# Kernel tuning notes

Measured on AMD Instinct MI355X. Metric: run time of the kernel, lower is better.

Reference implementation:

```python
import jax, jax.numpy as jnp
import numpy as np

N_USERS = 60000
N_ITEMS = 40000
N = N_USERS + N_ITEMS   # ncount
EMB = 64
NNZ = 3200000           # nnz of sparse_norm_adj (avg degree 32)
LN_EPS = 1e-5


def setup_inputs() -> dict:
    key = jax.random.key(0)
    ks = jax.random.split(key, 12)
    ego = jax.random.normal(ks[0], (N, EMB), jnp.float32) * 0.1
    rows = jax.random.randint(ks[1], (NNZ,), 0, N)
    cols = jax.random.randint(ks[2], (NNZ,), 0, N)
    # normalized adjacency values (non-trainable buffer)
    vals = jax.random.uniform(ks[3], (NNZ,), jnp.float32) * 0.01
    # xavier-uniform-ish scale for [64,64]: sqrt(2/(64+64)) = 0.125
    w_uu = jax.random.normal(ks[4], (EMB, EMB), jnp.float32) * 0.125
    filt_uu = jax.random.uniform(ks[5], (N_USERS,), jnp.float32, 0.99, 1.01)
    par_uu = jax.random.uniform(ks[6], (2,), jnp.float32, 0.0, 0.99)
    w_ii = jax.random.normal(ks[7], (EMB, EMB), jnp.float32) * 0.125
    filt_ii = jax.random.uniform(ks[8], (N_ITEMS,), jnp.float32, 0.99, 1.01)
    par_ii = jax.random.uniform(ks[9], (2,), jnp.float32, 0.0, 0.99)
    ln_gamma = jnp.ones((EMB,), jnp.float32)
    ln_beta = jnp.zeros((EMB,), jnp.float32)
    return {"ego_embeddings": ego, "rows": rows, "cols": cols, "vals": vals,
            "w_uu": w_uu, "filt_uu": filt_uu, "par_uu": par_uu,
            "w_ii": w_ii, "filt_ii": filt_ii, "par_ii": par_ii,
            "ln_gamma": ln_gamma, "ln_beta": ln_beta}


def _spmm(rows, cols, vals, x):
    # out[rows] += vals * x[cols]  <=>  sparse_adj @ x
    return jax.ops.segment_sum(vals[:, None] * x[cols], rows, num_segments=N)


def reference(ego_embeddings, rows, cols, vals, w_uu, filt_uu, par_uu,
              w_ii, filt_ii, par_ii, ln_gamma, ln_beta):
    res = ego_embeddings
    u = ego_embeddings[:N_USERS]
    it = ego_embeddings[N_USERS:]
    # HWNN layer with K1=K2=1 collapses to par0*par1 * diag(filter) @ X @ W
    user_ego = par_uu[0] * par_uu[1] * ((filt_uu[:, None] * u) @ w_uu) + u
    item_ego = par_ii[0] * par_ii[1] * ((filt_ii[:, None] * it) @ w_ii) + it
    ego = jnp.concatenate([user_ego, item_ego], axis=0)  # [N, EMB]
    # HGCNConv (act=False): adj @ (adj.T @ ego)
    h = jax.ops.segment_sum(vals[:, None] * ego[rows], cols, num_segments=N)  # adj.T @ ego
    y = _spmm(rows, cols, vals, h)                                            # adj @ h
    # LayerNorm (eps=1e-5, affine) + residual from the ORIGINAL input
    mu = jnp.mean(y, axis=-1, keepdims=True)
    var = jnp.var(y, axis=-1, keepdims=True)
    yn = (y - mu) / jnp.sqrt(var + LN_EPS) * ln_gamma + ln_beta
    out = yn + res
    return out[:N_USERS], out[N_USERS:]
```

## Files before the change

kernel.cpp:

```cpp
#include <hip/hip_runtime.h>

#define N_USERS 60000
#define N_ITEMS 40000
#define N_TOTAL 100000
#define EMB 64
#define LN_EPS 1e-5f

#define KPS 128
#define KSH 7
#define NSUP ((N_TOTAL + KPS - 1) / KPS)
#define EPB 4096
#define BLT 512
#define TR_ROWS 32
#define XPITCH 68
#define CAP 2048
#define SPT 512

__device__ __forceinline__ float bf2f(unsigned short h)
{ return __uint_as_float(((unsigned)h) << 16); }
__device__ __forceinline__ unsigned short f2bf(float f)
{
    unsigned u = __float_as_uint(f);
    return (unsigned short)((u + 0x7FFFu + ((u >> 16) & 1u)) >> 16);
}

__global__ void transform_tile(const float* __restrict__ x,
                               const float* __restrict__ w_uu,
                               const float* __restrict__ filt_uu,
                               const float* __restrict__ par_uu,
                               const float* __restrict__ w_ii,
                               const float* __restrict__ filt_ii,
                               const float* __restrict__ par_ii,
                               unsigned short* __restrict__ out)
{
    __shared__ float Wls[EMB * EMB];
    __shared__ float xs[TR_ROWS * XPITCH];
    const int tid = threadIdx.x;
    const int r0 = blockIdx.x * TR_ROWS;
    const int itm = (r0 >= N_USERS);
    const float* W  = itm ? w_ii : w_uu;
    const float* fb = itm ? filt_ii : filt_uu;
    const int foff  = itm ? N_USERS : 0;
    const float c   = itm ? par_ii[0] * par_ii[1] : par_uu[0] * par_uu[1];

    for (int i = tid; i < EMB * EMB / 4; i += 256)
        ((float4*)Wls)[i] = ((const float4*)W)[i];
    for (int i = tid; i < TR_ROWS * 16; i += 256) {
        const float4 v = ((const float4*)x)[r0 * 16 + i];
        *(float4*)&xs[(i >> 4) * XPITCH + (i & 15) * 4] = v;
    }
    __syncthreads();

    const int lane = tid & 63;
    const int wv = tid >> 6;
    const int rg = lane >> 4;
    const int j  = lane & 15;

#pragma unroll
    for (int it = 0; it < 2; ++it) {
        const int rl = wv * 8 + it * 4 + rg;
        const int row = r0 + rl;
        float4 acc = make_float4(0.f, 0.f, 0.f, 0.f);
#pragma unroll 8
        for (int k = 0; k < EMB; ++k) {
            const float xb = xs[rl * XPITCH + k];
            const float4 w4 = *(const float4*)&Wls[k * EMB + 4 * j];
            acc.x += xb * w4.x; acc.y += xb * w4.y;
            acc.z += xb * w4.z; acc.w += xb * w4.w;
        }
        const float cf = c * fb[row - foff];
        const float4 xv = *(const float4*)&xs[rl * XPITCH + 4 * j];
        ushort4 o;
        o.x = f2bf(cf * acc.x + xv.x);
        o.y = f2bf(cf * acc.y + xv.y);
        o.z = f2bf(cf * acc.z + xv.z);
        o.w = f2bf(cf * acc.w + xv.w);
        *(ushort4*)&out[(size_t)row * EMB + 4 * j] = o;
    }
}

__global__ void hist_sup(const int* __restrict__ rows,
                         const int* __restrict__ cols,
                         int* __restrict__ cnt_r,
                         int* __restrict__ cnt_c, int nnz)
{
    __shared__ int hr[NSUP], hc[NSUP];
    const int tid = threadIdx.x;
    for (int i = tid; i < NSUP; i += 256) { hr[i] = 0; hc[i] = 0; }
    __syncthreads();
    for (int e = blockIdx.x * 256 + tid; e < nnz; e += gridDim.x * 256) {
        atomicAdd(&hr[rows[e] >> KSH], 1);
        atomicAdd(&hc[cols[e] >> KSH], 1);
    }
    __syncthreads();
    for (int i = tid; i < NSUP; i += 256) {
        if (hr[i]) atomicAdd(&cnt_r[i], hr[i]);
        if (hc[i]) atomicAdd(&cnt_c[i], hc[i]);
    }
}

__global__ void scan_sup(const int* __restrict__ cnt_c, int* __restrict__ base_c,
                         int* __restrict__ cur_c,
                         const int* __restrict__ cnt_r, int* __restrict__ base_r,
                         int* __restrict__ cur_r)
{
    const int* cnt = blockIdx.x ? cnt_r : cnt_c;
    int* base = blockIdx.x ? base_r : base_c;
    int* cur  = blockIdx.x ? cur_r  : cur_c;
    __shared__ int wsum[16];
    const int i = threadIdx.x;
    const int lane = i & 63;
    const int wv = i >> 6;
    const int v = (i < NSUP) ? cnt[i] : 0;
    int incl = v;
#pragma unroll
    for (int off = 1; off < 64; off <<= 1) {
        const int t = __shfl_up(incl, off, 64);
        if (lane >= off) incl += t;
    }
    if (lane == 63) wsum[wv] = incl;
    __syncthreads();
    if (i == 0) {
        int run = 0;
#pragma unroll
        for (int w = 0; w < 16; ++w) { const int t = wsum[w]; wsum[w] = run; run += t; }
        base[NSUP] = run;
    }
    __syncthreads();
    const int excl = wsum[wv] + incl - v;
    if (i < NSUP) { base[i] = excl; cur[i] = excl; }
}

__global__ void __launch_bounds__(BLT, 6)
build_l1(const int* __restrict__ key,
         const int* __restrict__ other,
         const float* __restrict__ vals,
         int* __restrict__ cursor,
         int2* __restrict__ pairs1, int nnz)
{
    __shared__ int2 stage[EPB];
    __shared__ unsigned short sg[EPB];
    __shared__ int hist[NSUP];
    __shared__ int gbase[NSUP];
    __shared__ int lcur[NSUP];
    __shared__ int wsum[8];

    const int tid = threadIdx.x;
    const int e0 = blockIdx.x * EPB;
    const int ecnt = min(EPB, nnz - e0);

    for (int i = tid; i < NSUP; i += BLT) hist[i] = 0;
    __syncthreads();

    int myk[EPB / BLT], myo[EPB / BLT];
    float myv[EPB / BLT];
#pragma unroll
    for (int i = 0; i < EPB / BLT; ++i) {
        const int s = tid + i * BLT;
        if (s < ecnt) {
            const int e = e0 + s;
            myk[i] = key[e]; myo[i] = other[e]; myv[i] = vals[e];
            atomicAdd(&hist[myk[i] >> KSH], 1);
        } else myk[i] = -1;
    }
    __syncthreads();

    {
        const int lane = tid & 63;
        const int wv = tid >> 6;
        const int i0 = tid * 2;
        const int va = (i0     < NSUP) ? hist[i0]     : 0;
        const int vb = (i0 + 1 < NSUP) ? hist[i0 + 1] : 0;
        const int tsum = va + vb;
        int incl = tsum;
#pragma unroll
        for (int off = 1; off < 64; off <<= 1) {
            const int t = __shfl_up(incl, off, 64);
            if (lane >= off) incl += t;
        }
        if (lane == 63) wsum[wv] = incl;
        __syncthreads();
        int woff = 0;
        for (int w = 0; w < wv; ++w) woff += wsum[w];
        const int excl = woff + incl - tsum;
        if (i0 < NSUP) {
            lcur[i0] = excl;
            gbase[i0] = va ? atomicAdd(&cursor[i0], va) : 0;
            hist[i0] = excl;
        }
        if (i0 + 1 < NSUP) {
            lcur[i0 + 1] = excl + va;
            gbase[i0 + 1] = vb ? atomicAdd(&cursor[i0 + 1], vb) : 0;
            hist[i0 + 1] = excl + va;
        }
    }
    __syncthreads();

#pragma unroll
    for (int i = 0; i < EPB / BLT; ++i) {
        if (myk[i] >= 0) {
            const int g = myk[i] >> KSH;
            const int s = atomicAdd(&lcur[g], 1);
            stage[s] = make_int2(myo[i] | ((myk[i] & (KPS - 1)) << 20),
                                 __float_as_int(myv[i]));
            sg[s] = (unsigned short)g;
        }
    }
    __syncthreads();

    for (int s = tid; s < ecnt; s += BLT) {
        const int g = sg[s];
        pairs1[gbase[g] + (s - hist[g])] = stage[s];
    }
}

template <bool LN>
__global__ void __launch_bounds__(SPT, 6)
spmm_fused(const int* __restrict__ base,
           const int2* __restrict__ pairs,
           const unsigned short* __restrict__ src,
           const float* __restrict__ ego,
           const float* __restrict__ gamma,
           const float* __restrict__ beta,
           unsigned short* __restrict__ dstb,
           float* __restrict__ dstf)
{
    __shared__ int2 stage[CAP];
    __shared__ int2 sorted[CAP];
    __shared__ int cnt[KPS];
    __shared__ int kbase[KPS];
    __shared__ int kcur[KPS];

    const int tid = threadIdx.x;
    const int sup = blockIdx.x;
    const int beg = base[sup];
    const int end = base[sup + 1];
    const int g = tid >> 4;
    const int l = tid & 15;

    float4 acc[4];
#pragma unroll
    for (int i = 0; i < 4; ++i) acc[i] = make_float4(0.f, 0.f, 0.f, 0.f);

    if (tid < KPS) cnt[tid] = 0;
    __syncthreads();

    int c0 = beg;
    int csz = min(CAP, end - c0);
    for (int i = tid; i < csz; i += SPT) {
        const int2 v = pairs[c0 + i];
        stage[i] = v;
        atomicAdd(&cnt[(v.x >> 20) & (KPS - 1)], 1);
    }
    __syncthreads();

    while (csz > 0) {
        if (tid < 64) {
            const int ca = cnt[tid * 2];
            const int cb = cnt[tid * 2 + 1];
            const int tsum = ca + cb;
            int incl = tsum;
#pragma unroll
            for (int off = 1; off < 64; off <<= 1) {
                const int t = __shfl_up(incl, off, 64);
                if (tid >= off) incl += t;
            }
            const int run = incl - tsum;
            kbase[tid * 2] = run;          kcur[tid * 2] = run;
            kbase[tid * 2 + 1] = run + ca; kcur[tid * 2 + 1] = run + ca;
            cnt[tid * 2] = 0; cnt[tid * 2 + 1] = 0;
        }
        __syncthreads();

        for (int i = tid; i < csz; i += SPT) {
            const int2 v = stage[i];
            const int pos = atomicAdd(&kcur[(v.x >> 20) & (KPS - 1)], 1);
            sorted[pos] = v;
        }
        __syncthreads();

        const int nc0 = c0 + csz;
        const int ncsz = min(CAP, end - nc0);

#pragma unroll
        for (int rr = 0; rr < 4; ++rr) {
            const int k = g * 4 + rr;
            int j = kbase[k];
            const int e = kcur[k];
            float4 a = acc[rr];
            for (; j + 4 <= e; j += 4) {
                const int2 p0 = sorted[j];
                const int2 p1 = sorted[j + 1];
                const int2 p2 = sorted[j + 2];
                const int2 p3 = sorted[j + 3];
                const ushort4 s0 = ((const ushort4*)(src + (size_t)(p0.x & 0x1FFFF) * EMB))[l];
                const ushort4 s1 = ((const ushort4*)(src + (size_t)(p1.x & 0x1FFFF) * EMB))[l];
                const ushort4 s2 = ((const ushort4*)(src + (size_t)(p2.x & 0x1FFFF) * EMB))[l];
                const ushort4 s3 = ((const ushort4*)(src + (size_t)(p3.x & 0x1FFFF) * EMB))[l];
                const float v0 = __int_as_float(p0.y);
                const float v1 = __int_as_float(p1.y);
                const float v2 = __int_as_float(p2.y);
                const float v3 = __int_as_float(p3.y);
                a.x += v0 * bf2f(s0.x); a.y += v0 * bf2f(s0.y);
                a.z += v0 * bf2f(s0.z); a.w += v0 * bf2f(s0.w);
                a.x += v1 * bf2f(s1.x); a.y += v1 * bf2f(s1.y);
                a.z += v1 * bf2f(s1.z); a.w += v1 * bf2f(s1.w);
                a.x += v2 * bf2f(s2.x); a.y += v2 * bf2f(s2.y);
                a.z += v2 * bf2f(s2.z); a.w += v2 * bf2f(s2.w);
                a.x += v3 * bf2f(s3.x); a.y += v3 * bf2f(s3.y);
                a.z += v3 * bf2f(s3.z); a.w += v3 * bf2f(s3.w);
            }
            for (; j < e; ++j) {
                const int2 p = sorted[j];
                const ushort4 s = ((const ushort4*)(src + (size_t)(p.x & 0x1FFFF) * EMB))[l];
                const float v = __int_as_float(p.y);
                a.x += v * bf2f(s.x); a.y += v * bf2f(s.y);
                a.z += v * bf2f(s.z); a.w += v * bf2f(s.w);
            }
            acc[rr] = a;
        }

        for (int i = tid; i < ncsz; i += SPT) {
            const int2 v = pairs[nc0 + i];
            stage[i] = v;
            atomicAdd(&cnt[(v.x >> 20) & (KPS - 1)], 1);
        }
        c0 = nc0; csz = ncsz;
        __syncthreads();
    }

    const int r0 = sup * KPS + g * 4;
    if (!LN) {
#pragma unroll
        for (int rr = 0; rr < 4; ++rr) {
            const int row = r0 + rr;
            if (row < N_TOTAL) {
                ushort4 o;
                o.x = f2bf(acc[rr].x); o.y = f2bf(acc[rr].y);
                o.z = f2bf(acc[rr].z); o.w = f2bf(acc[rr].w);
                ((ushort4*)dstb)[(size_t)row * 16 + l] = o;
            }
        }
    } else {
        const float4 gm = ((const float4*)gamma)[l];
        const float4 bt = ((const float4*)beta)[l];
#pragma unroll
        for (int rr = 0; rr < 4; ++rr) {
            const int row = r0 + rr;
            const float4 a = acc[rr];
            float s  = a.x + a.y + a.z + a.w;
            float s2 = a.x * a.x + a.y * a.y + a.z * a.z + a.w * a.w;
#pragma unroll
            for (int m = 1; m <= 8; m <<= 1) {
                s  += __shfl_xor(s,  m, 64);
                s2 += __shfl_xor(s2, m, 64);
            }
            const float mu  = s * (1.0f / EMB);
            const float var = s2 * (1.0f / EMB) - mu * mu;
            const float inv = rsqrtf(var + LN_EPS);
            if (row < N_TOTAL) {
                const float4 eg = ((const float4*)(ego + (size_t)row * EMB))[l];
                float4 o;
                o.x = (a.x - mu) * inv * gm.x + bt.x + eg.x;
                o.y = (a.y - mu) * inv * gm.y + bt.y + eg.y;
                o.z = (a.z - mu) * inv * gm.z + bt.z + eg.z;
                o.w = (a.w - mu) * inv * gm.w + bt.w + eg.w;
                ((float4*)(dstf + (size_t)row * EMB))[l] = o;
            }
        }
    }
}

__global__ void transform_kernel(const float* __restrict__ x,
                                 const float* __restrict__ W,
                                 const float* __restrict__ filt,
                                 const float* __restrict__ par,
                                 float* __restrict__ out, int nrows)
{
    __shared__ float Ws[EMB * EMB];
    const int tid = threadIdx.x;
    for (int i = tid; i < EMB * EMB; i += blockDim.x) Ws[i] = W[i];
    __syncthreads();
    const float c = par[0] * par[1];
    const int lane = tid & 63;
    const int wave = tid >> 6;
    const int r0 = blockIdx.x * 32;
    for (int rr = wave; rr < 32; rr += 4) {
        const int r = r0 + rr;
        if (r >= nrows) break;
        const float xv = x[(size_t)r * EMB + lane];
        float acc = 0.f;
#pragma unroll
        for (int k = 0; k < EMB; ++k) {
            const float xk = __shfl(xv, k, 64);
            acc += xk * Ws[k * EMB + lane];
        }
        out[(size_t)r * EMB + lane] = c * filt[r] * acc + xv;
    }
}

__global__ void spmm_scatter(const int* __restrict__ src_idx,
                             const int* __restrict__ dst_idx,
                             const float* __restrict__ vals,
                             const float* __restrict__ src,
                             float* __restrict__ dst, int nnz)
{
    const long long t = (long long)blockIdx.x * blockDim.x + threadIdx.x;
    const int e = (int)(t >> 4);
    const int l = (int)(t & 15);
    if (e >= nnz) return;
    const int s = src_idx[e];
    const int d = dst_idx[e];
    const float v = vals[e];
    const float4 xv = ((const float4*)(src + (size_t)s * EMB))[l];
    float* dp = dst + (size_t)d * EMB + l * 4;
    atomicAdd(dp + 0, v * xv.x);
    atomicAdd(dp + 1, v * xv.y);
    atomicAdd(dp + 2, v * xv.z);
    atomicAdd(dp + 3, v * xv.w);
}

__global__ void ln_residual(const float* y,
                            const float* __restrict__ ego,
                            const float* __restrict__ gamma,
                            const float* __restrict__ beta,
                            float* out, int nrows)
{
    const int lane = threadIdx.x & 63;
    const int wave = threadIdx.x >> 6;
    const int r = blockIdx.x * 4 + wave;
    if (r >= nrows) return;
    const float v = y[(size_t)r * EMB + lane];
    float s = v, s2 = v * v;
#pragma unroll
    for (int off = 32; off > 0; off >>= 1) {
        s  += __shfl_down(s,  off, 64);
        s2 += __shfl_down(s2, off, 64);
    }
    s  = __shfl(s,  0, 64);
    s2 = __shfl(s2, 0, 64);
    const float mu  = s * (1.0f / EMB);
    const float var = s2 * (1.0f / EMB) - mu * mu;
    const float inv = rsqrtf(var + LN_EPS);
    out[(size_t)r * EMB + lane] =
        (v - mu) * inv * gamma[lane] + beta[lane] + ego[(size_t)r * EMB + lane];
}

extern "C" void kernel_launch(void* const* d_in, const int* in_sizes, int n_in,
                              void* d_out, int out_size, void* d_ws, size_t ws_size,
                              hipStream_t stream)
{
    const float* ego     = (const float*)d_in[0];
    const int*   rows    = (const int*)  d_in[1];
    const int*   cols    = (const int*)  d_in[2];
    const float* vals    = (const float*)d_in[3];
    const float* w_uu    = (const float*)d_in[4];
    const float* filt_uu = (const float*)d_in[5];
    const float* par_uu  = (const float*)d_in[6];
    const float* w_ii    = (const float*)d_in[7];
    const float* filt_ii = (const float*)d_in[8];
    const float* par_ii  = (const float*)d_in[9];
    const float* gamma   = (const float*)d_in[10];
    const float* beta    = (const float*)d_in[11];
    float* out = (float*)d_out;
    const int nnz = in_sizes[1];

    const size_t emb_elems = (size_t)N_TOTAL * EMB;
    const size_t emb_bytes = emb_elems * sizeof(float);
    const size_t bf_bytes  = emb_elems * sizeof(unsigned short);

    const size_t need = 2 * bf_bytes + (size_t)nnz * sizeof(int2)
                        + (size_t)(6 * (NSUP + 1)) * sizeof(int);

    if (ws_size >= need) {
        unsigned short* ego2b = (unsigned short*)d_ws;
        unsigned short* hb    = ego2b + emb_elems;
        int2* pairs1 = (int2*)(hb + emb_elems);
        int*  cnt_c  = (int*)(pairs1 + nnz);
        int*  cnt_r  = cnt_c + NSUP;
        int*  base_c = cnt_r + NSUP;
        int*  cur_c  = base_c + (NSUP + 1);
        int*  base_r = cur_c + NSUP;
        int*  cur_r  = base_r + (NSUP + 1);

        hipMemsetAsync(cnt_c, 0, 2 * NSUP * sizeof(int), stream);

        hist_sup<<<512, 256, 0, stream>>>(rows, cols, cnt_r, cnt_c, nnz);
        scan_sup<<<2, 1024, 0, stream>>>(cnt_c, base_c, cur_c,
                                         cnt_r, base_r, cur_r);

        transform_tile<<<N_TOTAL / TR_ROWS, 256, 0, stream>>>(
            ego, w_uu, filt_uu, par_uu, w_ii, filt_ii, par_ii, ego2b);

        const int l1b = (nnz + EPB - 1) / EPB;

        build_l1<<<l1b, BLT, 0, stream>>>(cols, rows, vals, cur_c, pairs1, nnz);
        spmm_fused<false><<<NSUP, SPT, 0, stream>>>(
            base_c, pairs1, ego2b, nullptr, nullptr, nullptr, hb, nullptr);

        build_l1<<<l1b, BLT, 0, stream>>>(rows, cols, vals, cur_r, pairs1, nnz);
        spmm_fused<true><<<NSUP, SPT, 0, stream>>>(
            base_r, pairs1, hb, ego, gamma, beta, nullptr, out);
    } else {
        float* ego2 = (float*)d_ws;
        float* h    = ego2 + emb_elems;
        hipMemsetAsync(h,   0, emb_bytes, stream);
        hipMemsetAsync(out, 0, emb_bytes, stream);

        transform_kernel<<<(N_USERS + 31) / 32, 256, 0, stream>>>(
            ego, w_uu, filt_uu, par_uu, ego2, N_USERS);
        transform_kernel<<<(N_ITEMS + 31) / 32, 256, 0, stream>>>(
            ego + (size_t)N_USERS * EMB, w_ii, filt_ii, par_ii,
            ego2 + (size_t)N_USERS * EMB, N_ITEMS);

        const long long thr = (long long)nnz * 16;
        const int sblocks = (int)((thr + 255) / 256);
        spmm_scatter<<<sblocks, 256, 0, stream>>>(rows, cols, vals, ego2, h, nnz);
        spmm_scatter<<<sblocks, 256, 0, stream>>>(cols, rows, vals, h, out, nnz);

        const int rb = (N_TOTAL + 3) / 4;
        ln_residual<<<rb, 256, 0, stream>>>(out, ego, gamma, beta, out, N_TOTAL);
    }
}
```

Measured before the change: 431.7 us.

## Build both column- and row-bucketed pair lists in one pass; unroll gather by 8

The two bucketing kernels (by column and by row) are merged into one kernel that reads rows/cols/vals once and writes two separate pair arrays, so the COO input is read once instead of twice. The workspace now holds both pair arrays, and launch bounds drop to 3 blocks per SM because the kernel needs an extra shared histogram and more registers. The SpMM inner loop gains an 8-way unrolled gather path so more independent loads are in flight per thread. This may raise register pressure. It also doubles the pair storage written to memory.

```diff
diff --git a/kernel.cpp b/kernel.cpp
--- a/kernel.cpp
+++ b/kernel.cpp
@@ -131,16 +131,17 @@
     if (i < NSUP) { base[i] = excl; cur[i] = excl; }
 }
 
-__global__ void __launch_bounds__(BLT, 6)
-build_l1(const int* __restrict__ key,
-         const int* __restrict__ other,
-         const float* __restrict__ vals,
-         int* __restrict__ cursor,
-         int2* __restrict__ pairs1, int nnz)
+__global__ void __launch_bounds__(BLT, 3)
+build_both(const int* __restrict__ rows,
+           const int* __restrict__ cols,
+           const float* __restrict__ vals,
+           int* __restrict__ cur_c, int2* __restrict__ pairs_c,
+           int* __restrict__ cur_r, int2* __restrict__ pairs_r, int nnz)
 {
     __shared__ int2 stage[EPB];
     __shared__ unsigned short sg[EPB];
-    __shared__ int hist[NSUP];
+    __shared__ int hist_c[NSUP];
+    __shared__ int hist_r[NSUP];
     __shared__ int gbase[NSUP];
     __shared__ int lcur[NSUP];
     __shared__ int wsum[8];
@@ -149,68 +150,79 @@
     const int e0 = blockIdx.x * EPB;
     const int ecnt = min(EPB, nnz - e0);
 
-    for (int i = tid; i < NSUP; i += BLT) hist[i] = 0;
-    __syncthreads();
-
-    int myk[EPB / BLT], myo[EPB / BLT];
+    for (int i = tid; i < NSUP; i += BLT) { hist_c[i] = 0; hist_r[i] = 0; }
+    __syncthreads();
+
+    int myr[EPB / BLT], myc[EPB / BLT];
     float myv[EPB / BLT];
 #pragma unroll
     for (int i = 0; i < EPB / BLT; ++i) {
         const int s = tid + i * BLT;
         if (s < ecnt) {
             const int e = e0 + s;
-            myk[i] = key[e]; myo[i] = other[e]; myv[i] = vals[e];
-            atomicAdd(&hist[myk[i] >> KSH], 1);
-        } else myk[i] = -1;
-    }
-    __syncthreads();
-
-    {
-        const int lane = tid & 63;
-        const int wv = tid >> 6;
-        const int i0 = tid * 2;
-        const int va = (i0     < NSUP) ? hist[i0]     : 0;
-        const int vb = (i0 + 1 < NSUP) ? hist[i0 + 1] : 0;
-        const int tsum = va + vb;
-        int incl = tsum;
-#pragma unroll
-        for (int off = 1; off < 64; off <<= 1) {
-            const int t = __shfl_up(incl, off, 64);
-            if (lane >= off) incl += t;
-        }
-        if (lane == 63) wsum[wv] = incl;
+            myr[i] = rows[e]; myc[i] = cols[e]; myv[i] = vals[e];
+            atomicAdd(&hist_c[myc[i] >> KSH], 1);
+            atomicAdd(&hist_r[myr[i] >> KSH], 1);
+        } else myr[i] = -1;
+    }
+    __syncthreads();
+
+#pragma unroll 1
+    for (int p = 0; p < 2; ++p) {
+        int* hist = p ? hist_r : hist_c;
+        int* gcur = p ? cur_r  : cur_c;
+        int2* out = p ? pairs_r : pairs_c;
+
+        {
+            const int lane = tid & 63;
+            const int wv = tid >> 6;
+            const int i0 = tid * 2;
+            const int va = (i0     < NSUP) ? hist[i0]     : 0;
+            const int vb = (i0 + 1 < NSUP) ? hist[i0 + 1] : 0;
+            const int tsum = va + vb;
+            int incl = tsum;
+#pragma unroll
+            for (int off = 1; off < 64; off <<= 1) {
+                const int t = __shfl_up(incl, off, 64);
+                if (lane >= off) incl += t;
+            }
+            if (lane == 63) wsum[wv] = incl;
+            __syncthreads();
+            int woff = 0;
+            for (int w = 0; w < wv; ++w) woff += wsum[w];
+            const int excl = woff + incl - tsum;
+            if (i0 < NSUP) {
+                lcur[i0] = excl;
+                gbase[i0] = va ? atomicAdd(&gcur[i0], va) : 0;
+                hist[i0] = excl;
+            }
+            if (i0 + 1 < NSUP) {
+                lcur[i0 + 1] = excl + va;
+                gbase[i0 + 1] = vb ? atomicAdd(&gcur[i0 + 1], vb) : 0;
+                hist[i0 + 1] = excl + va;
+            }
+        }
         __syncthreads();
-        int woff = 0;
-        for (int w = 0; w < wv; ++w) woff += wsum[w];
-        const int excl = woff + incl - tsum;
-        if (i0 < NSUP) {
-            lcur[i0] = excl;
-            gbase[i0] = va ? atomicAdd(&cursor[i0], va) : 0;
-            hist[i0] = excl;
-        }
-        if (i0 + 1 < NSUP) {
-            lcur[i0 + 1] = excl + va;
-            gbase[i0 + 1] = vb ? atomicAdd(&cursor[i0 + 1], vb) : 0;
-            hist[i0 + 1] = excl + va;
-        }
-    }
-    __syncthreads();
-
-#pragma unroll
-    for (int i = 0; i < EPB / BLT; ++i) {
-        if (myk[i] >= 0) {
-            const int g = myk[i] >> KSH;
-            const int s = atomicAdd(&lcur[g], 1);
-            stage[s] = make_int2(myo[i] | ((myk[i] & (KPS - 1)) << 20),
-                                 __float_as_int(myv[i]));
-            sg[s] = (unsigned short)g;
-        }
-    }
-    __syncthreads();
-
-    for (int s = tid; s < ecnt; s += BLT) {
-        const int g = sg[s];
-        pairs1[gbase[g] + (s - hist[g])] = stage[s];
+
+#pragma unroll
+        for (int i = 0; i < EPB / BLT; ++i) {
+            if (myr[i] >= 0) {
+                const int key   = p ? myr[i] : myc[i];
+                const int other = p ? myc[i] : myr[i];
+                const int g = key >> KSH;
+                const int s = atomicAdd(&lcur[g], 1);
+                stage[s] = make_int2(other | ((key & (KPS - 1)) << 20),
+                                     __float_as_int(myv[i]));
+                sg[s] = (unsigned short)g;
+            }
+        }
+        __syncthreads();
+
+        for (int s = tid; s < ecnt; s += BLT) {
+            const int g = sg[s];
+            out[gbase[g] + (s - hist[g])] = stage[s];
+        }
+        __syncthreads();
     }
 }
 
@@ -288,27 +300,33 @@
             int j = kbase[k];
             const int e = kcur[k];
             float4 a = acc[rr];
+            for (; j + 8 <= e; j += 8) {
+                int2 p[8]; ushort4 s[8];
+#pragma unroll
+                for (int u = 0; u < 8; ++u) p[u] = sorted[j + u];
+#pragma unroll
+                for (int u = 0; u < 8; ++u)
+                    s[u] = ((const ushort4*)(src + (size_t)(p[u].x & 0x1FFFF) * EMB))[l];
+#pragma unroll
+                for (int u = 0; u < 8; ++u) {
+                    const float v = __int_as_float(p[u].y);
+                    a.x += v * bf2f(s[u].x); a.y += v * bf2f(s[u].y);
+                    a.z += v * bf2f(s[u].z); a.w += v * bf2f(s[u].w);
+                }
+            }
             for (; j + 4 <= e; j += 4) {
-                const int2 p0 = sorted[j];
-                const int2 p1 = sorted[j + 1];
-                const int2 p2 = sorted[j + 2];
-                const int2 p3 = sorted[j + 3];
-                const ushort4 s0 = ((const ushort4*)(src + (size_t)(p0.x & 0x1FFFF) * EMB))[l];
-                const ushort4 s1 = ((const ushort4*)(src + (size_t)(p1.x & 0x1FFFF) * EMB))[l];
-                const ushort4 s2 = ((const ushort4*)(src + (size_t)(p2.x & 0x1FFFF) * EMB))[l];
-                const ushort4 s3 = ((const ushort4*)(src + (size_t)(p3.x & 0x1FFFF) * EMB))[l];
-                const float v0 = __int_as_float(p0.y);
-                const float v1 = __int_as_float(p1.y);
-                const float v2 = __int_as_float(p2.y);
-                const float v3 = __int_as_float(p3.y);
-                a.x += v0 * bf2f(s0.x); a.y += v0 * bf2f(s0.y);
-                a.z += v0 * bf2f(s0.z); a.w += v0 * bf2f(s0.w);
-                a.x += v1 * bf2f(s1.x); a.y += v1 * bf2f(s1.y);
-                a.z += v1 * bf2f(s1.z); a.w += v1 * bf2f(s1.w);
-                a.x += v2 * bf2f(s2.x); a.y += v2 * bf2f(s2.y);
-                a.z += v2 * bf2f(s2.z); a.w += v2 * bf2f(s2.w);
-                a.x += v3 * bf2f(s3.x); a.y += v3 * bf2f(s3.y);
-                a.z += v3 * bf2f(s3.z); a.w += v3 * bf2f(s3.w);
+                int2 p[4]; ushort4 s[4];
+#pragma unroll
+                for (int u = 0; u < 4; ++u) p[u] = sorted[j + u];
+#pragma unroll
+                for (int u = 0; u < 4; ++u)
+                    s[u] = ((const ushort4*)(src + (size_t)(p[u].x & 0x1FFFF) * EMB))[l];
+#pragma unroll
+                for (int u = 0; u < 4; ++u) {
+                    const float v = __int_as_float(p[u].y);
+                    a.x += v * bf2f(s[u].x); a.y += v * bf2f(s[u].y);
+                    a.z += v * bf2f(s[u].z); a.w += v * bf2f(s[u].w);
+                }
             }
             for (; j < e; ++j) {
                 const int2 p = sorted[j];
@@ -469,14 +487,15 @@
     const size_t emb_bytes = emb_elems * sizeof(float);
     const size_t bf_bytes  = emb_elems * sizeof(unsigned short);
 
-    const size_t need = 2 * bf_bytes + (size_t)nnz * sizeof(int2)
+    const size_t need = 2 * bf_bytes + 2 * (size_t)nnz * sizeof(int2)
                         + (size_t)(6 * (NSUP + 1)) * sizeof(int);
 
     if (ws_size >= need) {
         unsigned short* ego2b = (unsigned short*)d_ws;
         unsigned short* hb    = ego2b + emb_elems;
-        int2* pairs1 = (int2*)(hb + emb_elems);
-        int*  cnt_c  = (int*)(pairs1 + nnz);
+        int2* pairs_c = (int2*)(hb + emb_elems);
+        int2* pairs_r = pairs_c + nnz;
+        int*  cnt_c  = (int*)(pairs_r + nnz);
         int*  cnt_r  = cnt_c + NSUP;
         int*  base_c = cnt_r + NSUP;
         int*  cur_c  = base_c + (NSUP + 1);
@@ -493,14 +512,14 @@
             ego, w_uu, filt_uu, par_uu, w_ii, filt_ii, par_ii, ego2b);
 
         const int l1b = (nnz + EPB - 1) / EPB;
-
-        build_l1<<<l1b, BLT, 0, stream>>>(cols, rows, vals, cur_c, pairs1, nnz);
+        build_both<<<l1b, BLT, 0, stream>>>(rows, cols, vals,
+                                            cur_c, pairs_c, cur_r, pairs_r, nnz);
+
         spmm_fused<false><<<NSUP, SPT, 0, stream>>>(
-            base_c, pairs1, ego2b, nullptr, nullptr, nullptr, hb, nullptr);
-
-        build_l1<<<l1b, BLT, 0, stream>>>(rows, cols, vals, cur_r, pairs1, nnz);
+            base_c, pairs_c, ego2b, nullptr, nullptr, nullptr, hb, nullptr);
+
         spmm_fused<true><<<NSUP, SPT, 0, stream>>>(
-            base_r, pairs1, hb, ego, gamma, beta, nullptr, out);
+            base_r, pairs_r, hb, ego, gamma, beta, nullptr, out);
     } else {
         float* ego2 = (float*)d_ws;
         float* h    = ego2 + emb_elems;
```

After: 405.8 us. 6.0% less time.
